# Kernel optimization log

Measured on AMD Instinct MI355X. Metric: run time of the kernel, lower is better.

## Reference

```python
import jax, jax.numpy as jnp
import numpy as np

N_STEPS = 8          # spatial_interval
SPATIAL_SCALE = 1.0  # spatial_scale


def setup_inputs() -> dict:
    key = jax.random.key(0)
    ks = jax.random.split(key, 6)
    B, N, D = 32, 1024, 256
    x = jax.random.normal(ks[0], (B, N, D), dtype=jnp.float32)
    adj_mx = jax.random.uniform(ks[1], (N, N), dtype=jnp.float32) / N  # row-scaled dense adjacency
    alpha_train = jnp.ones((N,), dtype=jnp.float32)          # alpha * ones(num_node), alpha=1.0
    w = jnp.eye(D, dtype=jnp.float32) + 0.01 * jax.random.normal(ks[2], (D, D), dtype=jnp.float32)
    d = jax.random.uniform(ks[3], (D,), dtype=jnp.float32)
    fc_in_w = jax.random.normal(ks[4], (D, D), dtype=jnp.float32) * (1.0 / np.sqrt(D))
    fc_in_b = jnp.zeros((D,), dtype=jnp.float32)
    return {"x": x, "adj_mx": adj_mx, "alpha_train": alpha_train, "w": w,
            "d": d, "fc_in_w": fc_in_w, "fc_in_b": fc_in_b, "vt": 0}


def reference(x, adj_mx, alpha_train, w, d, fc_in_w, fc_in_b, vt):
    # x: [B, N, D]. x0 is detached in torch (x.clone().detach()).
    x0 = jax.lax.stop_gradient(x)
    # fc_in (dropout is identity in eval mode)
    h = jnp.einsum('bnd,ed->bne', x, fc_in_w) + fc_in_b
    # constants of the diffusion ODE
    alph = jax.nn.sigmoid(alpha_train)[:, None]          # [N, 1]
    d_clamped = jnp.clip(d, 0.0, 1.0)
    w_eff = (w * d_clamped) @ w.T                        # [D, D]
    dt = jnp.float32(SPATIAL_SCALE / N_STEPS)

    def euler_step(h, _):
        ax = jnp.einsum('nm,bmd->bnd', adj_mx, h)        # graph diffusion
        f = alph * 0.5 * (ax - h) + h @ w_eff - h + x0
        return h + dt * f, None

    h, _ = jax.lax.scan(euler_step, h, None, length=N_STEPS)
    return h
```

## Files before the change

### kernel.cpp

```cpp
#include <hip/hip_runtime.h>
#include <hip/hip_bf16.h>
#include <stdint.h>

typedef __bf16 bf16;
typedef __bf16 bf16x8 __attribute__((ext_vector_type(8)));
typedef __bf16 bf16x4 __attribute__((ext_vector_type(4)));
typedef float f32x4 __attribute__((ext_vector_type(4)));


__device__ __forceinline__ void gload_lds16(const bf16* g, bf16* l) {
    __builtin_amdgcn_global_load_lds(
        (const __attribute__((address_space(1))) void*)g,
        (__attribute__((address_space(3))) void*)l, 16, 0, 0);
}

__device__ __forceinline__ void stageA(const bf16* __restrict__ g, int lda,
                                       bf16* l, int t) {
#pragma unroll
    for (int i = 0; i < 4; ++i) {
        int c = (i << 8) + t;
        int row = c >> 3, slot = c & 7;
        gload_lds16(g + (size_t)row * lda + ((slot ^ (row & 7)) << 3), l + c * 8);
    }
}
__device__ __forceinline__ void stageB(const bf16* __restrict__ g, int ldb,
                                       bf16* l, int t) {
#pragma unroll
    for (int i = 0; i < 2; ++i) {
        int c = (i << 8) + t;
        int row = c >> 3, slot = c & 7;
        gload_lds16(g + (size_t)row * ldb + ((slot ^ (row & 7)) << 3), l + c * 8);
    }
}

__device__ __forceinline__ void mma_tile(const bf16* A, const bf16* B,
                                         f32x4 acc[2][4], int lane, int wv) {
    const int r0 = wv * 32 + (lane & 15);
    const int kq = lane >> 4;
    bf16x8 a[2][2], b[4][2];
#pragma unroll
    for (int mi = 0; mi < 2; ++mi) {
        int rA = r0 + mi * 16;
#pragma unroll
        for (int kk = 0; kk < 2; ++kk) {
            int kc = kk * 4 + kq;
            a[mi][kk] = *(const bf16x8*)&A[rA * 64 + ((kc ^ (rA & 7)) << 3)];
        }
    }
#pragma unroll
    for (int ni = 0; ni < 4; ++ni) {
        int rB = ni * 16 + (lane & 15);
#pragma unroll
        for (int kk = 0; kk < 2; ++kk) {
            int kc = kk * 4 + kq;
            b[ni][kk] = *(const bf16x8*)&B[rB * 64 + ((kc ^ (rB & 7)) << 3)];
        }
    }
#pragma unroll
    for (int kk = 0; kk < 2; ++kk)
#pragma unroll
        for (int mi = 0; mi < 2; ++mi)
#pragma unroll
            for (int ni = 0; ni < 4; ++ni)
                acc[mi][ni] = __builtin_amdgcn_mfma_f32_16x16x32_bf16(
                    a[mi][kk], b[ni][kk], acc[mi][ni], 0, 0, 0);
}

template <int NT, typename F>
__device__ __forceinline__ void run_pipeline(F tadr, bf16 (*As)[8192],
                                             bf16 (*Bs)[4096], f32x4 acc[2][4],
                                             int t, int lane, int wv) {
    {
        const bf16 *Ag, *Bg; int lda, ldb;
        tadr(0, Ag, lda, Bg, ldb);
        stageA(Ag, lda, As[0], t);
        stageB(Bg, ldb, Bs[0], t);
    }
#pragma unroll 1
    for (int i = 0; i < NT; ++i) {
        if (i + 1 < NT) {
            const bf16 *Ag, *Bg; int lda, ldb;
            tadr(i + 1, Ag, lda, Bg, ldb);
            stageA(Ag, lda, As[(i + 1) & 1], t);
            stageB(Bg, ldb, Bs[(i + 1) & 1], t);
            asm volatile("s_waitcnt vmcnt(6)" ::: "memory");
        } else {
            asm volatile("s_waitcnt vmcnt(0)" ::: "memory");
        }
        __builtin_amdgcn_s_barrier();
        asm volatile("" ::: "memory");
        mma_tile(As[i & 1], Bs[i & 1], acc, lane, wv);
        asm volatile("" ::: "memory");
        __builtin_amdgcn_s_barrier();
    }
}

__global__ void prep_alpha(const float* __restrict__ a, float* __restrict__ out) {
    int i = blockIdx.x * blockDim.x + threadIdx.x;
    if (i < 1024) out[i] = 0.5f / (1.0f + __expf(-a[i]));
}

__global__ void prep_adj(const float* __restrict__ adj, const float* __restrict__ ahs,
                         bf16* __restrict__ adjb) {
    int i = blockIdx.x * blockDim.x + threadIdx.x;
    int row = i >> 8;
    float s = ahs[row];
    float4 v = ((const float4*)adj)[i];
    bf16x4 o = {(bf16)(s * v.x), (bf16)(s * v.y), (bf16)(s * v.z), (bf16)(s * v.w)};
    ((bf16x4*)adjb)[i] = o;
}

__global__ void cast_f32_bf16x4(const float* __restrict__ src, bf16* __restrict__ dst,
                                int n4) {
    int i = blockIdx.x * blockDim.x + threadIdx.x;
    if (i < n4) {
        float4 v = ((const float4*)src)[i];
        bf16x4 o = {(bf16)v.x, (bf16)v.y, (bf16)v.z, (bf16)v.w};
        ((bf16x4*)dst)[i] = o;
    }
}

__global__ void prep_weff(const float* __restrict__ w, const float* __restrict__ dv,
                          bf16* __restrict__ weffT) {
    __shared__ float wk[256];
    __shared__ float dd[256];
    int k = blockIdx.x, j = threadIdx.x;
    dd[j] = fminf(fmaxf(dv[j], 0.0f), 1.0f);
    wk[j] = w[k * 256 + j];
    __syncthreads();
    float s = 0.0f;
#pragma unroll 8
    for (int c = 0; c < 256; ++c) s += wk[c] * dd[c] * w[j * 256 + c];
    weffT[j * 256 + k] = (bf16)s;
}

__launch_bounds__(256, 2)
__global__ void gemm_fcin(const bf16* __restrict__ xb, const bf16* __restrict__ fcwb,
                          const float* __restrict__ fcb, float* __restrict__ hf,
                          bf16* __restrict__ hb, bf16* __restrict__ hT) {
    __shared__ __align__(16) bf16 As[2][8192];
    __shared__ __align__(16) bf16 Bs[2][4096];
    int t = threadIdx.x, lane = t & 63, wv = t >> 6;
    int row0 = blockIdx.y * 128;
    int col0 = blockIdx.x * 64;
    f32x4 acc[2][4] = {};
    const bf16* Ab = xb + (size_t)row0 * 256;
    const bf16* Bb = fcwb + (size_t)col0 * 256;
    auto tadr = [&](int i, const bf16*& Ag, int& lda, const bf16*& Bg, int& ldb) {
        Ag = Ab + i * 64; lda = 256;
        Bg = Bb + i * 64; ldb = 256;
    };
    run_pipeline<4>(tadr, As, Bs, acc, t, lane, wv);

    int rbase = row0 + wv * 32 + ((lane >> 4) << 2);
    int cbase = col0 + (lane & 15);
#pragma unroll
    for (int mi = 0; mi < 2; ++mi) {
        int rg = rbase + mi * 16;
#pragma unroll
        for (int ni = 0; ni < 4; ++ni) {
            int col = cbase + ni * 16;
            float bias = fcb[col];
            bf16x4 tv;
#pragma unroll
            for (int r = 0; r < 4; ++r) {
                float v = acc[mi][ni][r] + bias;
                size_t idx = (size_t)(rg + r) * 256 + col;
                hf[idx] = v;
                bf16 vb = (bf16)v;
                hb[idx] = vb;
                tv[r] = vb;
            }
            int b = rg >> 10, n = rg & 1023;
            *(bf16x4*)&hT[(((size_t)(b * 256 + col)) << 10) + n] = tv;
        }
    }
}

__launch_bounds__(256, 2)
__global__ void gemm_step(const bf16* __restrict__ adjb, const bf16* __restrict__ hbp,
                          const bf16* __restrict__ hTp, const bf16* __restrict__ weffT,
                          const float* __restrict__ ahs, const bf16* __restrict__ x0b,
                          float* __restrict__ hf, bf16* __restrict__ hbn,
                          bf16* __restrict__ hTn) {
    __shared__ __align__(16) bf16 As[2][8192];
    __shared__ __align__(16) bf16 Bs[2][4096];
    int t = threadIdx.x, lane = t & 63, wv = t >> 6;
    int g = blockIdx.x;
    int xcd = g & 7, rest = g >> 3;
    int xy = rest & 31;
    int b = (rest >> 5) * 8 + xcd;
    int d0 = (xy & 3) * 64;
    int n0 = (xy >> 2) * 128;
    f32x4 acc[2][4] = {};

    const bf16* A1 = adjb + (size_t)n0 * 1024;
    const bf16* B1 = hTp + ((size_t)(b * 256 + d0)) * 1024;
    const bf16* A2 = hbp + ((size_t)(b * 1024 + n0)) * 256;
    const bf16* B2 = weffT + (size_t)d0 * 256;
    auto tadr = [&](int i, const bf16*& Ag, int& lda, const bf16*& Bg, int& ldb) {
        if (i < 16) {
            Ag = A1 + i * 64; lda = 1024;
            Bg = B1 + i * 64; ldb = 1024;
        } else {
            Ag = A2 + (i - 16) * 64; lda = 256;
            Bg = B2 + (i - 16) * 64; ldb = 256;
        }
    };
    run_pipeline<20>(tadr, As, Bs, acc, t, lane, wv);

    const float dt = 0.125f;
    int rb = wv * 32 + ((lane >> 4) << 2);
    int cb = d0 + (lane & 15);
#pragma unroll
    for (int mi = 0; mi < 2; ++mi) {
        int nr = n0 + rb + mi * 16;
#pragma unroll
        for (int ni = 0; ni < 4; ++ni) {
            int col = cb + ni * 16;
            bf16x4 tv;
#pragma unroll
            for (int r = 0; r < 4; ++r) {
                int node = nr + r;
                size_t idx = (((size_t)b << 10) + node) * 256 + col;
                float hold = hf[idx];
                float x0v = (float)x0b[idx];
                float f = acc[mi][ni][r] - (ahs[node] + 1.0f) * hold + x0v;
                float hv = hold + dt * f;
                hf[idx] = hv;
                bf16 vb = (bf16)hv;
                hbn[idx] = vb;
                tv[r] = vb;
            }
            *(bf16x4*)&hTn[(((size_t)(b * 256 + col)) << 10) + nr] = tv;
        }
    }
}

extern "C" void kernel_launch(void* const* d_in, const int* in_sizes, int n_in,
                              void* d_out, int out_size, void* d_ws, size_t ws_size,
                              hipStream_t stream) {
    const float* x     = (const float*)d_in[0];
    const float* adj   = (const float*)d_in[1];
    const float* alpha = (const float*)d_in[2];
    const float* w     = (const float*)d_in[3];
    const float* dvec  = (const float*)d_in[4];
    const float* fcw   = (const float*)d_in[5];
    const float* fcb   = (const float*)d_in[6];
    float* out = (float*)d_out;

    const size_t HB = (size_t)32 * 1024 * 256 * 2;
    char* p = (char*)d_ws;
    bf16* hb0   = (bf16*)p; p += HB;
    bf16* hb1   = (bf16*)p; p += HB;
    bf16* hT0   = (bf16*)p; p += HB;
    bf16* hT1   = (bf16*)p; p += HB;
    bf16* xb    = (bf16*)p; p += HB;
    bf16* adjb  = (bf16*)p; p += (size_t)1024 * 1024 * 2;
    bf16* fcwb  = (bf16*)p; p += 256 * 256 * 2;
    bf16* weffT = (bf16*)p; p += 256 * 256 * 2;
    float* ahs  = (float*)p; p += 1024 * 4;

    prep_alpha<<<4, 256, 0, stream>>>(alpha, ahs);
    prep_adj<<<1024, 256, 0, stream>>>(adj, ahs, adjb);
    prep_weff<<<256, 256, 0, stream>>>(w, dvec, weffT);
    cast_f32_bf16x4<<<8192, 256, 0, stream>>>(x, xb, 2097152);
    cast_f32_bf16x4<<<64, 256, 0, stream>>>(fcw, fcwb, 16384);

    gemm_fcin<<<dim3(4, 256), 256, 0, stream>>>(xb, fcwb, fcb, out, hb0, hT0);

    bf16* hb[2] = {hb0, hb1};
    bf16* hT[2] = {hT0, hT1};
    int cur = 0;
    for (int s = 0; s < 8; ++s) {
        gemm_step<<<1024, 256, 0, stream>>>(
            adjb, hb[cur], hT[cur], weffT, ahs, xb, out, hb[cur ^ 1], hT[cur ^ 1]);
        cur ^= 1;
    }
}
```

Measured before the change: 457.2 us.

## Triple-buffer GEMM pipeline and store fp32 state as split bf16 hi/lo

The GEMM main loop moves from double to triple buffering in LDS with a two-tile prefetch distance and wave priority raised around the MFMA block. This aims to hide global-load latency better. The fp32 running state is replaced by a bf16 hi part plus a bf16 lo residual, which cuts per-step epilogue traffic from a 4-byte read and write to two 2-byte reads and writes. Only the last step writes fp32 output. The extra LDS (72KB per block) may lower occupancy below the two blocks per CU the launch bounds request. The lo buffer is updated in place within a step, which is safe because each element is read and written by the same thread.

Result: no change. 450.9 us (-1.4%).

```diff
diff --git a/kernel.cpp b/kernel.cpp
--- a/kernel.cpp
+++ b/kernel.cpp
@@ -75,23 +75,33 @@
         tadr(0, Ag, lda, Bg, ldb);
         stageA(Ag, lda, As[0], t);
         stageB(Bg, ldb, Bs[0], t);
-    }
+        if (NT > 1) {
+            tadr(1, Ag, lda, Bg, ldb);
+            stageA(Ag, lda, As[1], t);
+            stageB(Bg, ldb, Bs[1], t);
+        }
+    }
+    int cur = 0, pre = 2;
 #pragma unroll 1
     for (int i = 0; i < NT; ++i) {
-        if (i + 1 < NT) {
+        if (i + 2 < NT) {
             const bf16 *Ag, *Bg; int lda, ldb;
-            tadr(i + 1, Ag, lda, Bg, ldb);
-            stageA(Ag, lda, As[(i + 1) & 1], t);
-            stageB(Bg, ldb, Bs[(i + 1) & 1], t);
+            tadr(i + 2, Ag, lda, Bg, ldb);
+            stageA(Ag, lda, As[pre], t);
+            stageB(Bg, ldb, Bs[pre], t);
+            asm volatile("s_waitcnt vmcnt(12)" ::: "memory");
+        } else if (i + 1 < NT) {
             asm volatile("s_waitcnt vmcnt(6)" ::: "memory");
         } else {
             asm volatile("s_waitcnt vmcnt(0)" ::: "memory");
         }
         __builtin_amdgcn_s_barrier();
-        asm volatile("" ::: "memory");
-        mma_tile(As[i & 1], Bs[i & 1], acc, lane, wv);
-        asm volatile("" ::: "memory");
+        __builtin_amdgcn_s_setprio(1);
+        mma_tile(As[cur], Bs[cur], acc, lane, wv);
+        __builtin_amdgcn_s_setprio(0);
         __builtin_amdgcn_s_barrier();
+        cur = (cur == 2) ? 0 : cur + 1;
+        pre = (pre == 2) ? 0 : pre + 1;
     }
 }
 
@@ -136,10 +146,11 @@
 
 __launch_bounds__(256, 2)
 __global__ void gemm_fcin(const bf16* __restrict__ xb, const bf16* __restrict__ fcwb,
-                          const float* __restrict__ fcb, float* __restrict__ hf,
-                          bf16* __restrict__ hb, bf16* __restrict__ hT) {
-    __shared__ __align__(16) bf16 As[2][8192];
-    __shared__ __align__(16) bf16 Bs[2][4096];
+                          const float* __restrict__ fcb,
+                          bf16* __restrict__ hb, bf16* __restrict__ hT,
+                          bf16* __restrict__ hlo) {
+    __shared__ __align__(16) bf16 As[3][8192];
+    __shared__ __align__(16) bf16 Bs[3][4096];
     int t = threadIdx.x, lane = t & 63, wv = t >> 6;
     int row0 = blockIdx.y * 128;
     int col0 = blockIdx.x * 64;
@@ -166,10 +177,11 @@
             for (int r = 0; r < 4; ++r) {
                 float v = acc[mi][ni][r] + bias;
                 size_t idx = (size_t)(rg + r) * 256 + col;
-                hf[idx] = v;
-                bf16 vb = (bf16)v;
-                hb[idx] = vb;
-                tv[r] = vb;
+                bf16 hi = (bf16)v;
+                bf16 lo = (bf16)(v - (float)hi);
+                hb[idx] = hi;
+                hlo[idx] = lo;
+                tv[r] = hi;
             }
             int b = rg >> 10, n = rg & 1023;
             *(bf16x4*)&hT[(((size_t)(b * 256 + col)) << 10) + n] = tv;
@@ -177,14 +189,15 @@
     }
 }
 
+template <bool LAST>
 __launch_bounds__(256, 2)
 __global__ void gemm_step(const bf16* __restrict__ adjb, const bf16* __restrict__ hbp,
                           const bf16* __restrict__ hTp, const bf16* __restrict__ weffT,
                           const float* __restrict__ ahs, const bf16* __restrict__ x0b,
-                          float* __restrict__ hf, bf16* __restrict__ hbn,
-                          bf16* __restrict__ hTn) {
-    __shared__ __align__(16) bf16 As[2][8192];
-    __shared__ __align__(16) bf16 Bs[2][4096];
+                          bf16* __restrict__ hlo, bf16* __restrict__ hbn,
+                          bf16* __restrict__ hTn, float* __restrict__ out) {
+    __shared__ __align__(16) bf16 As[3][8192];
+    __shared__ __align__(16) bf16 Bs[3][4096];
     int t = threadIdx.x, lane = t & 63, wv = t >> 6;
     int g = blockIdx.x;
     int xcd = g & 7, rest = g >> 3;
@@ -223,16 +236,24 @@
             for (int r = 0; r < 4; ++r) {
                 int node = nr + r;
                 size_t idx = (((size_t)b << 10) + node) * 256 + col;
-                float hold = hf[idx];
+                float hi = (float)hbp[idx];
+                float lo = (float)hlo[idx];
+                float hold = hi + lo;
                 float x0v = (float)x0b[idx];
                 float f = acc[mi][ni][r] - (ahs[node] + 1.0f) * hold + x0v;
                 float hv = hold + dt * f;
-                hf[idx] = hv;
-                bf16 vb = (bf16)hv;
-                hbn[idx] = vb;
-                tv[r] = vb;
+                if (LAST) {
+                    out[idx] = hv;
+                } else {
+                    bf16 nhi = (bf16)hv;
+                    bf16 nlo = (bf16)(hv - (float)nhi);
+                    hbn[idx] = nhi;
+                    hlo[idx] = nlo;
+                    tv[r] = nhi;
+                }
             }
-            *(bf16x4*)&hTn[(((size_t)(b * 256 + col)) << 10) + nr] = tv;
+            if (!LAST)
+                *(bf16x4*)&hTn[(((size_t)(b * 256 + col)) << 10) + nr] = tv;
         }
     }
 }
@@ -256,6 +277,7 @@
     bf16* hT0   = (bf16*)p; p += HB;
     bf16* hT1   = (bf16*)p; p += HB;
     bf16* xb    = (bf16*)p; p += HB;
+    bf16* hlo   = (bf16*)p; p += HB;
     bf16* adjb  = (bf16*)p; p += (size_t)1024 * 1024 * 2;
     bf16* fcwb  = (bf16*)p; p += 256 * 256 * 2;
     bf16* weffT = (bf16*)p; p += 256 * 256 * 2;
@@ -267,14 +289,20 @@
     cast_f32_bf16x4<<<8192, 256, 0, stream>>>(x, xb, 2097152);
     cast_f32_bf16x4<<<64, 256, 0, stream>>>(fcw, fcwb, 16384);
 
-    gemm_fcin<<<dim3(4, 256), 256, 0, stream>>>(xb, fcwb, fcb, out, hb0, hT0);
+    gemm_fcin<<<dim3(4, 256), 256, 0, stream>>>(xb, fcwb, fcb, hb0, hT0, hlo);
 
     bf16* hb[2] = {hb0, hb1};
     bf16* hT[2] = {hT0, hT1};
     int cur = 0;
     for (int s = 0; s < 8; ++s) {
-        gemm_step<<<1024, 256, 0, stream>>>(
-            adjb, hb[cur], hT[cur], weffT, ahs, xb, out, hb[cur ^ 1], hT[cur ^ 1]);
+        if (s < 7)
+            gemm_step<false><<<1024, 256, 0, stream>>>(
+                adjb, hb[cur], hT[cur], weffT, ahs, xb, hlo,
+                hb[cur ^ 1], hT[cur ^ 1], out);
+        else
+            gemm_step<true><<<1024, 256, 0, stream>>>(
+                adjb, hb[cur], hT[cur], weffT, ahs, xb, hlo,
+                hb[cur ^ 1], hT[cur ^ 1], out);
         cur ^= 1;
     }
 }
```
